# Kernel optimization log

Measured on AMD Instinct MI355X. Metric: run time of the kernel, lower is better.

The kernel has to match this reference:

```python
import jax, jax.numpy as jnp
import numpy as np

D_IN = 1024
D_OUT = 1024
N_HEADS = 16
HEAD_DIM = D_OUT // N_HEADS


def setup_inputs() -> dict:
    key = jax.random.key(0)
    ks = jax.random.split(key, 5)
    scale = 0.02
    x = jax.random.normal(ks[0], (2, 2048, D_IN), dtype=jnp.float32)
    Wq = jax.random.normal(ks[1], (D_IN, D_OUT), dtype=jnp.float32) * scale
    Wk = jax.random.normal(ks[2], (D_IN, D_OUT), dtype=jnp.float32) * scale
    Wv = jax.random.normal(ks[3], (D_IN, D_OUT), dtype=jnp.float32) * scale
    Wout = jax.random.normal(ks[4], (D_OUT, D_OUT), dtype=jnp.float32) * scale
    return {"x": x, "Wq": Wq, "Wk": Wk, "Wv": Wv, "Wout": Wout}


def reference(x, Wq, Wk, Wv, Wout):
    batch, seq_len, _ = x.shape
    # projections (no bias)
    Q = (x @ Wq).reshape(batch, seq_len, N_HEADS, HEAD_DIM)
    K = (x @ Wk).reshape(batch, seq_len, N_HEADS, HEAD_DIM)
    V = (x @ Wv).reshape(batch, seq_len, N_HEADS, HEAD_DIM)
    # scores: [batch, heads, seq, seq]
    scores = jnp.einsum("bqhd,bkhd->bhqk", Q, K) / jnp.sqrt(
        jnp.asarray(HEAD_DIM, dtype=x.dtype)
    )
    # causal mask: positions k > q masked to -inf
    causal = jnp.tril(jnp.ones((seq_len, seq_len), dtype=bool))
    scores = jnp.where(causal[None, None], scores, -jnp.inf)
    weights = jax.nn.softmax(scores, axis=-1)
    vectors = jnp.einsum("bhqk,bkhd->bqhd", weights, V)
    vectors = vectors.reshape(batch, seq_len, D_OUT)
    return vectors @ Wout
```

## Files before the change

kernel.cpp:

```cpp
#include <hip/hip_runtime.h>
#include <hip/hip_bf16.h>


typedef __attribute__((ext_vector_type(8))) _Float16 vhalf8;
typedef __attribute__((ext_vector_type(4))) _Float16 vhalf4;
typedef __attribute__((ext_vector_type(4))) float vfloat4;

#define D_MODEL 1024
#define SEQ     2048
#define NB      2
#define NH      16
#define HD      64

#define SCALE_K1 0.18033688f

__device__ __forceinline__ void async16(const void* g, void* l) {
  __builtin_amdgcn_global_load_lds(
      (const __attribute__((address_space(1))) unsigned int*)g,
      (__attribute__((address_space(3))) unsigned int*)l, 16, 0, 0);
}

__global__ __launch_bounds__(256) void prep(
    const float* __restrict__ x,
    const float* __restrict__ Wq, const float* __restrict__ Wk,
    const float* __restrict__ Wv, const float* __restrict__ Wo,
    _Float16* __restrict__ Xh, _Float16* __restrict__ Wt_qkv,
    _Float16* __restrict__ Wot) {
  int z = blockIdx.z;
  int t = threadIdx.x;
  if (z == 4) {
    int id = blockIdx.y * 16 + blockIdx.x;
#pragma unroll
    for (int pass = 0; pass < 8; pass++) {
      size_t i = ((size_t)(pass * 256 + id) * 256 + t) * 8;
      float4 a = *(const float4*)&x[i];
      float4 b = *(const float4*)&x[i + 4];
      vhalf8 h;
      h[0] = (_Float16)a.x; h[1] = (_Float16)a.y;
      h[2] = (_Float16)a.z; h[3] = (_Float16)a.w;
      h[4] = (_Float16)b.x; h[5] = (_Float16)b.y;
      h[6] = (_Float16)b.z; h[7] = (_Float16)b.w;
      *(vhalf8*)&Xh[i] = h;
    }
    return;
  }
  __shared__ _Float16 tile[64][65];
  const float* in = (z == 0) ? Wq : (z == 1) ? Wk : (z == 2) ? Wv : Wo;
  _Float16* out = (z < 3) ? (Wt_qkv + (size_t)z * 1024 * 1024) : Wot;
  int c0 = blockIdx.x * 64, r0 = blockIdx.y * 64;
  int tc = t & 63, tr = t >> 6;
#pragma unroll
  for (int p = 0; p < 16; p++) {
    int r = tr + p * 4;
    tile[r][tc] = (_Float16)in[(size_t)(r0 + r) * 1024 + c0 + tc];
  }
  __syncthreads();
#pragma unroll
  for (int p = 0; p < 16; p++) {
    int r = tr + p * 4;
    out[(size_t)(c0 + r) * 1024 + r0 + tc] = tile[tc][r];
  }
}

template <int BN>
__global__ __launch_bounds__(256) void gemm128(
    const _Float16* __restrict__ A, const _Float16* __restrict__ Bt,
    _Float16* __restrict__ Ch, float* __restrict__ Cf,
    _Float16* __restrict__ Vt, int M, int N, int K, int mode) {
  constexpr int ACH = 8;
  constexpr int BCH = BN / 16;
  constexpr int CPW = (ACH + BCH) / 4;
  constexpr int JN = BN / 32;
  __shared__ _Float16 As[128 * 32];
  __shared__ _Float16 Bs[BN * 32];
  int m0 = blockIdx.x * 128, n0 = blockIdx.y * BN;
  int t = threadIdx.x;
  int lane = t & 63, wave = t >> 6;
  int wm = (wave >> 1) * 64, wn = (wave & 1) * (BN / 2);
  int col = lane & 15, quad = lane >> 4;
  int srow = lane >> 2;
  int gcol = (((lane & 3) ^ (srow & 3)) << 3);

  vfloat4 acc[4][JN];
#pragma unroll
  for (int i = 0; i < 4; i++)
#pragma unroll
    for (int j = 0; j < JN; j++) {
      acc[i][j][0] = 0.f; acc[i][j][1] = 0.f;
      acc[i][j][2] = 0.f; acc[i][j][3] = 0.f;
    }

  int xq = (quad ^ (col & 3)) * 8;

  for (int k0 = 0; k0 < K; k0 += 32) {
    __syncthreads();
#pragma unroll
    for (int j = 0; j < CPW; j++) {
      int c = wave * CPW + j;
      if (c < ACH) {
        int row = c * 16 + srow;
        async16(&A[(size_t)(m0 + row) * K + k0 + gcol], &As[c * 512]);
      } else {
        int row = (c - ACH) * 16 + srow;
        async16(&Bt[(size_t)(n0 + row) * K + k0 + gcol], &Bs[(c - ACH) * 512]);
      }
    }
    __syncthreads();

    vhalf8 af[4], bf[JN];
#pragma unroll
    for (int i = 0; i < 4; i++)
      af[i] = *(const vhalf8*)&As[(wm + i * 16 + col) * 32 + xq];
#pragma unroll
    for (int j = 0; j < JN; j++)
      bf[j] = *(const vhalf8*)&Bs[(wn + j * 16 + col) * 32 + xq];
#pragma unroll
    for (int i = 0; i < 4; i++)
#pragma unroll
      for (int j = 0; j < JN; j++)
        acc[i][j] = __builtin_amdgcn_mfma_f32_16x16x32_f16(af[i], bf[j], acc[i][j], 0, 0, 0);
  }

  bool vmode = (mode == 2) && (n0 >= 2048);
#pragma unroll
  for (int i = 0; i < 4; i++)
#pragma unroll
    for (int j = 0; j < JN; j++) {
      if (vmode) {
        int n = n0 + wn + j * 16 + col;
        int nn = n - 2048;
        int hh = nn >> 6, dd = nn & 63;
        int m_base = m0 + wm + i * 16 + quad * 4;
        int bb = m_base >> 11, ss = m_base & 2047;
        vhalf4 pk;
        pk[0] = (_Float16)acc[i][j][0]; pk[1] = (_Float16)acc[i][j][1];
        pk[2] = (_Float16)acc[i][j][2]; pk[3] = (_Float16)acc[i][j][3];
        *(vhalf4*)&Vt[(((size_t)bb * NH + hh) * HD + dd) * SEQ + ss] = pk;
      } else {
#pragma unroll
        for (int r = 0; r < 4; r++) {
          int m = m0 + wm + i * 16 + quad * 4 + r;
          int n = n0 + wn + j * 16 + col;
          if (mode == 1)
            Cf[(size_t)m * N + n] = acc[i][j][r];
          else
            Ch[(size_t)m * N + n] = (_Float16)acc[i][j][r];
        }
      }
    }
}

__global__ __launch_bounds__(512) void attn(
    const _Float16* __restrict__ QKV, const _Float16* __restrict__ Vt,
    _Float16* __restrict__ Vec) {
  int blk = blockIdx.x;
  int pp = blk >> 5;
  int hb = blk & 31;
  int h = hb & 15;
  int b = hb >> 4;

  const _Float16* Qb  = QKV + (size_t)(b * SEQ) * 3072 + h * HD;
  const _Float16* Kb  = QKV + (size_t)(b * SEQ) * 3072 + 1024 + h * HD;
  const _Float16* Vtb = Vt + (size_t)(b * NH + h) * HD * SEQ;

  int t = threadIdx.x;
  int lane = t & 63, wave = t >> 6;
  int sw = wave & 3, hf = wave >> 2;
  int col = lane & 15, quad = lane >> 4;

  __shared__ _Float16 Ks[2][64][72];
  __shared__ _Float16 Vs[2][64][72];
  __shared__ _Float16 Ps[8][16][72];
  __shared__ float Om[64][65];
  __shared__ float Lm[64];

  int tl = t & 255;
  int srow = tl >> 2;
  int scol = (tl & 3) * 16;
  int kslot = ((srow & 3) << 4) + (srow >> 2);
  int kcol = scol ^ ((srow & 3) << 4);

  int tiles[2] = {31 - pp, pp};

  vhalf8 kr0, kr1, vr0, vr1;
  {
    const _Float16* kg = &Kb[(size_t)(hf * 64 + srow) * 3072 + scol];
    kr0 = *(const vhalf8*)kg; kr1 = *(const vhalf8*)(kg + 8);
    const _Float16* vg = &Vtb[(size_t)srow * SEQ + hf * 64 + scol];
    vr0 = *(const vhalf8*)vg; vr1 = *(const vhalf8*)(vg + 8);
  }

#pragma unroll
  for (int phase = 0; phase < 2; phase++) {
    int qt = tiles[phase];
    int q0 = qt * 64;
    int ntk = qt + 1;
    int J = (ntk + 1) >> 1;
    int wq0 = q0 + sw * 16;

    vhalf8 qf0 = *(const vhalf8*)&Qb[(size_t)(wq0 + col) * 3072 + quad * 8];
    vhalf8 qf1 = *(const vhalf8*)&Qb[(size_t)(wq0 + col) * 3072 + 32 + quad * 8];
#pragma unroll
    for (int i = 0; i < 8; i++) {
      qf0[i] = qf0[i] * (_Float16)SCALE_K1;
      qf1[i] = qf1[i] * (_Float16)SCALE_K1;
    }

    vfloat4 o[4];
#pragma unroll
    for (int i = 0; i < 4; i++) { o[i][0]=0.f; o[i][1]=0.f; o[i][2]=0.f; o[i][3]=0.f; }
    float lsum[4] = {0.f, 0.f, 0.f, 0.f};

    for (int j = 0; j < J; j++) {
      int ti = 2 * j + hf;
      bool active = (ti < ntk);
      int kb = ti * 64;
      if (active) {
        *(vhalf8*)&Ks[hf][kslot][kcol]     = kr0;
        *(vhalf8*)&Ks[hf][kslot][kcol + 8] = kr1;
        *(vhalf8*)&Vs[hf][srow][scol]      = vr0;
        *(vhalf8*)&Vs[hf][srow][scol + 8]  = vr1;
      }
      __syncthreads();

      {
        int tnext;
        if (phase == 0)
          tnext = (ti + 2 < ntk) ? (ti + 2) : hf;
        else
          tnext = (ti + 2 < ntk) ? (ti + 2) : ti;
        int kpf = tnext * 64;
        const _Float16* kg = &Kb[(size_t)(kpf + srow) * 3072 + scol];
        kr0 = *(const vhalf8*)kg; kr1 = *(const vhalf8*)(kg + 8);
        const _Float16* vg = &Vtb[(size_t)srow * SEQ + kpf + scol];
        vr0 = *(const vhalf8*)vg; vr1 = *(const vhalf8*)(vg + 8);
      }

      if (active) {
        vhalf8 kf[4][2];
#pragma unroll
        for (int hh = 0; hh < 4; hh++) {
          int swz = hh << 4;
          kf[hh][0] = *(const vhalf8*)&Ks[hf][hh * 16 + col][(quad * 8) ^ swz];
          kf[hh][1] = *(const vhalf8*)&Ks[hf][hh * 16 + col][(32 + quad * 8) ^ swz];
        }
        vfloat4 s[4];
#pragma unroll
        for (int hh = 0; hh < 4; hh++) {
          vfloat4 z; z[0]=0.f; z[1]=0.f; z[2]=0.f; z[3]=0.f;
          z = __builtin_amdgcn_mfma_f32_16x16x32_f16(qf0, kf[hh][0], z, 0, 0, 0);
          z = __builtin_amdgcn_mfma_f32_16x16x32_f16(qf1, kf[hh][1], z, 0, 0, 0);
          s[hh] = z;
        }
        bool diag = (kb + 63 > wq0);
#pragma unroll
        for (int r = 0; r < 4; r++) {
          int q = wq0 + quad * 4 + r;
          float p[4];
#pragma unroll
          for (int hh = 0; hh < 4; hh++) {
            float sc = s[hh][r];
            if (diag && (kb + 4 * col + hh > q)) sc = -1e30f;
            p[hh] = __builtin_exp2f(sc);
          }
          lsum[r] += (p[0] + p[1]) + (p[2] + p[3]);
          vhalf4 ph;
          ph[0] = (_Float16)p[0]; ph[1] = (_Float16)p[1];
          ph[2] = (_Float16)p[2]; ph[3] = (_Float16)p[3];
          *(vhalf4*)&Ps[wave][quad * 4 + r][4 * col] = ph;
        }
        __asm__ __volatile__("s_waitcnt lgkmcnt(0)" ::: "memory");
        vhalf8 pf0 = *(const vhalf8*)&Ps[wave][col][quad * 8];
        vhalf8 pf1 = *(const vhalf8*)&Ps[wave][col][32 + quad * 8];
#pragma unroll
        for (int tt = 0; tt < 4; tt++) {
          vhalf8 vf0 = *(const vhalf8*)&Vs[hf][tt * 16 + col][quad * 8];
          vhalf8 vf1 = *(const vhalf8*)&Vs[hf][tt * 16 + col][32 + quad * 8];
          o[tt] = __builtin_amdgcn_mfma_f32_16x16x32_f16(pf0, vf0, o[tt], 0, 0, 0);
          o[tt] = __builtin_amdgcn_mfma_f32_16x16x32_f16(pf1, vf1, o[tt], 0, 0, 0);
        }
      }
      __syncthreads();
    }

    float rs[4];
#pragma unroll
    for (int r = 0; r < 4; r++) {
      float v = lsum[r];
#pragma unroll
      for (int msk = 1; msk < 16; msk <<= 1) v += __shfl_xor(v, msk, 64);
      rs[r] = v;
    }
    if (hf == 1) {
#pragma unroll
      for (int tt = 0; tt < 4; tt++)
#pragma unroll
        for (int r = 0; r < 4; r++)
          Om[sw * 16 + quad * 4 + r][tt * 16 + col] = o[tt][r];
      if (col == 0)
#pragma unroll
        for (int r = 0; r < 4; r++)
          Lm[sw * 16 + quad * 4 + r] = rs[r];
    }
    __syncthreads();
    if (hf == 0) {
      float inv_l[4];
#pragma unroll
      for (int r = 0; r < 4; r++)
        inv_l[r] = 1.0f / (rs[r] + Lm[sw * 16 + quad * 4 + r]);
#pragma unroll
      for (int tt = 0; tt < 4; tt++)
#pragma unroll
        for (int r = 0; r < 4; r++) {
          int q = wq0 + quad * 4 + r;
          int d = tt * 16 + col;
          float ov = o[tt][r] + Om[sw * 16 + quad * 4 + r][tt * 16 + col];
          Vec[(size_t)(b * SEQ + q) * D_MODEL + h * HD + d] =
              (_Float16)(ov * inv_l[r]);
        }
    }
  }
}

extern "C" void kernel_launch(void* const* d_in, const int* in_sizes, int n_in,
                              void* d_out, int out_size, void* d_ws, size_t ws_size,
                              hipStream_t stream) {
  const float* x  = (const float*)d_in[0];
  const float* Wq = (const float*)d_in[1];
  const float* Wk = (const float*)d_in[2];
  const float* Wv = (const float*)d_in[3];
  const float* Wo = (const float*)d_in[4];
  float* out = (float*)d_out;

  char* ws = (char*)d_ws;
  _Float16* Xh     = (_Float16*)ws;
  _Float16* Wt_qkv = (_Float16*)(ws + 8388608);
  _Float16* Wot    = (_Float16*)(ws + 14680064);
  _Float16* QKV    = (_Float16*)(ws + 16777216);
  _Float16* Vt     = (_Float16*)(ws + 41943040);
  _Float16* Vec    = (_Float16*)(ws + 50331648);

  dim3 tb(256);
  prep<<<dim3(16, 16, 5), tb, 0, stream>>>(x, Wq, Wk, Wv, Wo, Xh, Wt_qkv, Wot);
  gemm128<128><<<dim3(32, 24), tb, 0, stream>>>(Xh, Wt_qkv, QKV, nullptr, Vt,
                                                4096, 3072, 1024, 2);
  attn<<<dim3(512), dim3(512), 0, stream>>>(QKV, Vt, Vec);
  gemm128<64><<<dim3(32, 16), tb, 0, stream>>>(Vec, Wot, nullptr, out, nullptr,
                                               4096, 1024, 1024, 1);
}
```

Baseline: 182.2 us.

## Halve attention block size, give each wave 32 query rows for K/V reuse

The attention kernel now runs 256 threads per block instead of 512. Each wave handles two 16-row query sub-tiles, so every K and V fragment read from LDS feeds twice as many MFMAs. The K tile buffer and the output-merge buffer now share LDS through a union to cut the footprint. In exchange, per-thread register pressure rises, each thread issues twice as many global loads, and an extra barrier is added between phases to protect the aliased LDS.

```diff
diff --git a/kernel.cpp b/kernel.cpp
--- a/kernel.cpp
+++ b/kernel.cpp
@@ -150,7 +150,7 @@
     }
 }
 
-__global__ __launch_bounds__(512) void attn(
+__global__ __launch_bounds__(256, 2) void attn(
     const _Float16* __restrict__ QKV, const _Float16* __restrict__ Vt,
     _Float16* __restrict__ Vec) {
   int blk = blockIdx.x;
@@ -165,29 +165,36 @@
 
   int t = threadIdx.x;
   int lane = t & 63, wave = t >> 6;
-  int sw = wave & 3, hf = wave >> 2;
+  int sw = wave & 1, hf = wave >> 1;
   int col = lane & 15, quad = lane >> 4;
 
-  __shared__ _Float16 Ks[2][64][72];
+  __shared__ union {
+    _Float16 Ks[2][64][72];
+    float    Om[64][65];
+  } su;
   __shared__ _Float16 Vs[2][64][72];
-  __shared__ _Float16 Ps[8][16][72];
-  __shared__ float Om[64][65];
+  __shared__ _Float16 Ps[4][32][72];
   __shared__ float Lm[64];
 
-  int tl = t & 255;
+  int tl = t & 127;
   int srow = tl >> 2;
   int scol = (tl & 3) * 16;
-  int kslot = ((srow & 3) << 4) + (srow >> 2);
+  int kslotA = ((srow & 3) << 4) + (srow >> 2);
+  int kslotB = kslotA + 8;
   int kcol = scol ^ ((srow & 3) << 4);
 
   int tiles[2] = {31 - pp, pp};
 
-  vhalf8 kr0, kr1, vr0, vr1;
+  vhalf8 krA0, krA1, krB0, krB1, vrA0, vrA1, vrB0, vrB1;
   {
     const _Float16* kg = &Kb[(size_t)(hf * 64 + srow) * 3072 + scol];
-    kr0 = *(const vhalf8*)kg; kr1 = *(const vhalf8*)(kg + 8);
+    krA0 = *(const vhalf8*)kg; krA1 = *(const vhalf8*)(kg + 8);
+    kg += (size_t)32 * 3072;
+    krB0 = *(const vhalf8*)kg; krB1 = *(const vhalf8*)(kg + 8);
     const _Float16* vg = &Vtb[(size_t)srow * SEQ + hf * 64 + scol];
-    vr0 = *(const vhalf8*)vg; vr1 = *(const vhalf8*)(vg + 8);
+    vrA0 = *(const vhalf8*)vg; vrA1 = *(const vhalf8*)(vg + 8);
+    vg += (size_t)32 * SEQ;
+    vrB0 = *(const vhalf8*)vg; vrB1 = *(const vhalf8*)(vg + 8);
   }
 
 #pragma unroll
@@ -196,30 +203,44 @@
     int q0 = qt * 64;
     int ntk = qt + 1;
     int J = (ntk + 1) >> 1;
-    int wq0 = q0 + sw * 16;
-
-    vhalf8 qf0 = *(const vhalf8*)&Qb[(size_t)(wq0 + col) * 3072 + quad * 8];
-    vhalf8 qf1 = *(const vhalf8*)&Qb[(size_t)(wq0 + col) * 3072 + 32 + quad * 8];
-#pragma unroll
-    for (int i = 0; i < 8; i++) {
-      qf0[i] = qf0[i] * (_Float16)SCALE_K1;
-      qf1[i] = qf1[i] * (_Float16)SCALE_K1;
-    }
-
-    vfloat4 o[4];
-#pragma unroll
-    for (int i = 0; i < 4; i++) { o[i][0]=0.f; o[i][1]=0.f; o[i][2]=0.f; o[i][3]=0.f; }
-    float lsum[4] = {0.f, 0.f, 0.f, 0.f};
+    int wq0 = q0 + sw * 32;
+
+    vhalf8 qf0[2], qf1[2];
+#pragma unroll
+    for (int qs = 0; qs < 2; qs++) {
+      const _Float16* qp = &Qb[(size_t)(wq0 + qs * 16 + col) * 3072 + quad * 8];
+      qf0[qs] = *(const vhalf8*)qp;
+      qf1[qs] = *(const vhalf8*)(qp + 32);
+#pragma unroll
+      for (int i = 0; i < 8; i++) {
+        qf0[qs][i] = qf0[qs][i] * (_Float16)SCALE_K1;
+        qf1[qs][i] = qf1[qs][i] * (_Float16)SCALE_K1;
+      }
+    }
+
+    vfloat4 o[2][4];
+#pragma unroll
+    for (int qs = 0; qs < 2; qs++)
+#pragma unroll
+      for (int i = 0; i < 4; i++) {
+        o[qs][i][0] = 0.f; o[qs][i][1] = 0.f;
+        o[qs][i][2] = 0.f; o[qs][i][3] = 0.f;
+      }
+    float lsum[2][4] = {{0.f, 0.f, 0.f, 0.f}, {0.f, 0.f, 0.f, 0.f}};
 
     for (int j = 0; j < J; j++) {
       int ti = 2 * j + hf;
       bool active = (ti < ntk);
       int kb = ti * 64;
       if (active) {
-        *(vhalf8*)&Ks[hf][kslot][kcol]     = kr0;
-        *(vhalf8*)&Ks[hf][kslot][kcol + 8] = kr1;
-        *(vhalf8*)&Vs[hf][srow][scol]      = vr0;
-        *(vhalf8*)&Vs[hf][srow][scol + 8]  = vr1;
+        *(vhalf8*)&su.Ks[hf][kslotA][kcol]     = krA0;
+        *(vhalf8*)&su.Ks[hf][kslotA][kcol + 8] = krA1;
+        *(vhalf8*)&su.Ks[hf][kslotB][kcol]     = krB0;
+        *(vhalf8*)&su.Ks[hf][kslotB][kcol + 8] = krB1;
+        *(vhalf8*)&Vs[hf][srow][scol]          = vrA0;
+        *(vhalf8*)&Vs[hf][srow][scol + 8]      = vrA1;
+        *(vhalf8*)&Vs[hf][srow + 32][scol]     = vrB0;
+        *(vhalf8*)&Vs[hf][srow + 32][scol + 8] = vrB1;
       }
       __syncthreads();
 
@@ -231,9 +252,13 @@
           tnext = (ti + 2 < ntk) ? (ti + 2) : ti;
         int kpf = tnext * 64;
         const _Float16* kg = &Kb[(size_t)(kpf + srow) * 3072 + scol];
-        kr0 = *(const vhalf8*)kg; kr1 = *(const vhalf8*)(kg + 8);
+        krA0 = *(const vhalf8*)kg; krA1 = *(const vhalf8*)(kg + 8);
+        kg += (size_t)32 * 3072;
+        krB0 = *(const vhalf8*)kg; krB1 = *(const vhalf8*)(kg + 8);
         const _Float16* vg = &Vtb[(size_t)srow * SEQ + kpf + scol];
-        vr0 = *(const vhalf8*)vg; vr1 = *(const vhalf8*)(vg + 8);
+        vrA0 = *(const vhalf8*)vg; vrA1 = *(const vhalf8*)(vg + 8);
+        vg += (size_t)32 * SEQ;
+        vrB0 = *(const vhalf8*)vg; vrB1 = *(const vhalf8*)(vg + 8);
       }
 
       if (active) {
@@ -241,84 +266,105 @@
 #pragma unroll
         for (int hh = 0; hh < 4; hh++) {
           int swz = hh << 4;
-          kf[hh][0] = *(const vhalf8*)&Ks[hf][hh * 16 + col][(quad * 8) ^ swz];
-          kf[hh][1] = *(const vhalf8*)&Ks[hf][hh * 16 + col][(32 + quad * 8) ^ swz];
-        }
-        vfloat4 s[4];
-#pragma unroll
-        for (int hh = 0; hh < 4; hh++) {
-          vfloat4 z; z[0]=0.f; z[1]=0.f; z[2]=0.f; z[3]=0.f;
-          z = __builtin_amdgcn_mfma_f32_16x16x32_f16(qf0, kf[hh][0], z, 0, 0, 0);
-          z = __builtin_amdgcn_mfma_f32_16x16x32_f16(qf1, kf[hh][1], z, 0, 0, 0);
-          s[hh] = z;
-        }
-        bool diag = (kb + 63 > wq0);
-#pragma unroll
-        for (int r = 0; r < 4; r++) {
-          int q = wq0 + quad * 4 + r;
-          float p[4];
+          kf[hh][0] = *(const vhalf8*)&su.Ks[hf][hh * 16 + col][(quad * 8) ^ swz];
+          kf[hh][1] = *(const vhalf8*)&su.Ks[hf][hh * 16 + col][(32 + quad * 8) ^ swz];
+        }
+#pragma unroll
+        for (int qs = 0; qs < 2; qs++) {
+          int wq = wq0 + qs * 16;
+          vfloat4 s[4];
 #pragma unroll
           for (int hh = 0; hh < 4; hh++) {
-            float sc = s[hh][r];
-            if (diag && (kb + 4 * col + hh > q)) sc = -1e30f;
-            p[hh] = __builtin_exp2f(sc);
+            vfloat4 z; z[0]=0.f; z[1]=0.f; z[2]=0.f; z[3]=0.f;
+            z = __builtin_amdgcn_mfma_f32_16x16x32_f16(qf0[qs], kf[hh][0], z, 0, 0, 0);
+            z = __builtin_amdgcn_mfma_f32_16x16x32_f16(qf1[qs], kf[hh][1], z, 0, 0, 0);
+            s[hh] = z;
           }
-          lsum[r] += (p[0] + p[1]) + (p[2] + p[3]);
-          vhalf4 ph;
-          ph[0] = (_Float16)p[0]; ph[1] = (_Float16)p[1];
-          ph[2] = (_Float16)p[2]; ph[3] = (_Float16)p[3];
-          *(vhalf4*)&Ps[wave][quad * 4 + r][4 * col] = ph;
+          bool diag = (kb + 63 > wq);
+#pragma unroll
+          for (int r = 0; r < 4; r++) {
+            int q = wq + quad * 4 + r;
+            float p[4];
+#pragma unroll
+            for (int hh = 0; hh < 4; hh++) {
+              float sc = s[hh][r];
+              if (diag && (kb + 4 * col + hh > q)) sc = -1e30f;
+              p[hh] = __builtin_exp2f(sc);
+            }
+            lsum[qs][r] += (p[0] + p[1]) + (p[2] + p[3]);
+            vhalf4 ph;
+            ph[0] = (_Float16)p[0]; ph[1] = (_Float16)p[1];
+            ph[2] = (_Float16)p[2]; ph[3] = (_Float16)p[3];
+            *(vhalf4*)&Ps[wave][qs * 16 + quad * 4 + r][4 * col] = ph;
+          }
         }
         __asm__ __volatile__("s_waitcnt lgkmcnt(0)" ::: "memory");
-        vhalf8 pf0 = *(const vhalf8*)&Ps[wave][col][quad * 8];
-        vhalf8 pf1 = *(const vhalf8*)&Ps[wave][col][32 + quad * 8];
+        vhalf8 pf0[2], pf1[2];
+#pragma unroll
+        for (int qs = 0; qs < 2; qs++) {
+          pf0[qs] = *(const vhalf8*)&Ps[wave][qs * 16 + col][quad * 8];
+          pf1[qs] = *(const vhalf8*)&Ps[wave][qs * 16 + col][32 + quad * 8];
+        }
 #pragma unroll
         for (int tt = 0; tt < 4; tt++) {
           vhalf8 vf0 = *(const vhalf8*)&Vs[hf][tt * 16 + col][quad * 8];
           vhalf8 vf1 = *(const vhalf8*)&Vs[hf][tt * 16 + col][32 + quad * 8];
-          o[tt] = __builtin_amdgcn_mfma_f32_16x16x32_f16(pf0, vf0, o[tt], 0, 0, 0);
-          o[tt] = __builtin_amdgcn_mfma_f32_16x16x32_f16(pf1, vf1, o[tt], 0, 0, 0);
+#pragma unroll
+          for (int qs = 0; qs < 2; qs++) {
+            o[qs][tt] = __builtin_amdgcn_mfma_f32_16x16x32_f16(pf0[qs], vf0, o[qs][tt], 0, 0, 0);
+            o[qs][tt] = __builtin_amdgcn_mfma_f32_16x16x32_f16(pf1[qs], vf1, o[qs][tt], 0, 0, 0);
+          }
         }
       }
       __syncthreads();
     }
 
-    float rs[4];
-#pragma unroll
-    for (int r = 0; r < 4; r++) {
-      float v = lsum[r];
-#pragma unroll
-      for (int msk = 1; msk < 16; msk <<= 1) v += __shfl_xor(v, msk, 64);
-      rs[r] = v;
-    }
+    float rs[2][4];
+#pragma unroll
+    for (int qs = 0; qs < 2; qs++)
+#pragma unroll
+      for (int r = 0; r < 4; r++) {
+        float v = lsum[qs][r];
+#pragma unroll
+        for (int msk = 1; msk < 16; msk <<= 1) v += __shfl_xor(v, msk, 64);
+        rs[qs][r] = v;
+      }
     if (hf == 1) {
 #pragma unroll
-      for (int tt = 0; tt < 4; tt++)
-#pragma unroll
-        for (int r = 0; r < 4; r++)
-          Om[sw * 16 + quad * 4 + r][tt * 16 + col] = o[tt][r];
-      if (col == 0)
-#pragma unroll
-        for (int r = 0; r < 4; r++)
-          Lm[sw * 16 + quad * 4 + r] = rs[r];
+      for (int qs = 0; qs < 2; qs++) {
+#pragma unroll
+        for (int tt = 0; tt < 4; tt++)
+#pragma unroll
+          for (int r = 0; r < 4; r++)
+            su.Om[sw * 32 + qs * 16 + quad * 4 + r][tt * 16 + col] = o[qs][tt][r];
+        if (col == 0)
+#pragma unroll
+          for (int r = 0; r < 4; r++)
+            Lm[sw * 32 + qs * 16 + quad * 4 + r] = rs[qs][r];
+      }
     }
     __syncthreads();
     if (hf == 0) {
-      float inv_l[4];
-#pragma unroll
-      for (int r = 0; r < 4; r++)
-        inv_l[r] = 1.0f / (rs[r] + Lm[sw * 16 + quad * 4 + r]);
-#pragma unroll
-      for (int tt = 0; tt < 4; tt++)
-#pragma unroll
-        for (int r = 0; r < 4; r++) {
-          int q = wq0 + quad * 4 + r;
-          int d = tt * 16 + col;
-          float ov = o[tt][r] + Om[sw * 16 + quad * 4 + r][tt * 16 + col];
-          Vec[(size_t)(b * SEQ + q) * D_MODEL + h * HD + d] =
-              (_Float16)(ov * inv_l[r]);
-        }
-    }
+#pragma unroll
+      for (int qs = 0; qs < 2; qs++) {
+        float inv_l[4];
+#pragma unroll
+        for (int r = 0; r < 4; r++)
+          inv_l[r] = 1.0f / (rs[qs][r] + Lm[sw * 32 + qs * 16 + quad * 4 + r]);
+#pragma unroll
+        for (int tt = 0; tt < 4; tt++)
+#pragma unroll
+          for (int r = 0; r < 4; r++) {
+            int q = wq0 + qs * 16 + quad * 4 + r;
+            int d = tt * 16 + col;
+            float ov = o[qs][tt][r] +
+                       su.Om[sw * 32 + qs * 16 + quad * 4 + r][tt * 16 + col];
+            Vec[(size_t)(b * SEQ + q) * D_MODEL + h * HD + d] =
+                (_Float16)(ov * inv_l[r]);
+          }
+      }
+    }
+    __syncthreads();
   }
 }
 
@@ -344,7 +390,7 @@
   prep<<<dim3(16, 16, 5), tb, 0, stream>>>(x, Wq, Wk, Wv, Wo, Xh, Wt_qkv, Wot);
   gemm128<128><<<dim3(32, 24), tb, 0, stream>>>(Xh, Wt_qkv, QKV, nullptr, Vt,
                                                 4096, 3072, 1024, 2);
-  attn<<<dim3(512), dim3(512), 0, stream>>>(QKV, Vt, Vec);
+  attn<<<dim3(512), dim3(256), 0, stream>>>(QKV, Vt, Vec);
   gemm128<64><<<dim3(32, 16), tb, 0, stream>>>(Vec, Wot, nullptr, out, nullptr,
                                                4096, 1024, 1024, 1);
 }
```

Result: slower. 197.1 us (+8.2%).

## Split attention into one block per query tile, drop KV split-merge

Applied to the files above, without the earlier changes.

The attention kernel no longer gives each 512-thread block a pair of query tiles (long plus short) with two wave halves splitting the key tiles and merging through shared memory. It now launches 1024 blocks of 256 threads, each handling a single query tile over all its key tiles, ordered longest-first in a zigzag to balance load. This removes the Om/Lm cross-half reduction and cuts shared memory, allowing more resident blocks per CU. The cost is a serial key loop per block with no intra-block split, and the loop runs twice as many iterations per wave.

```diff
diff --git a/kernel.cpp b/kernel.cpp
--- a/kernel.cpp
+++ b/kernel.cpp
@@ -150,176 +150,142 @@
     }
 }
 
-__global__ __launch_bounds__(512) void attn(
+__global__ __launch_bounds__(256, 4) void attn(
     const _Float16* __restrict__ QKV, const _Float16* __restrict__ Vt,
     _Float16* __restrict__ Vec) {
-  int blk = blockIdx.x;
-  int pp = blk >> 5;
-  int hb = blk & 31;
+  int g = blockIdx.x;
+  int qti = g >> 5;
+  int hb = g & 31;
   int h = hb & 15;
   int b = hb >> 4;
+  int jj = qti & 7, aa = qti >> 3;
+  int qt = (aa == 0) ? (31 - jj) : (aa == 1) ? (16 + jj)
+         : (aa == 2) ? (15 - jj) : jj;
 
   const _Float16* Qb  = QKV + (size_t)(b * SEQ) * 3072 + h * HD;
   const _Float16* Kb  = QKV + (size_t)(b * SEQ) * 3072 + 1024 + h * HD;
   const _Float16* Vtb = Vt + (size_t)(b * NH + h) * HD * SEQ;
 
   int t = threadIdx.x;
-  int lane = t & 63, wave = t >> 6;
-  int sw = wave & 3, hf = wave >> 2;
+  int lane = t & 63, sw = t >> 6;
   int col = lane & 15, quad = lane >> 4;
 
-  __shared__ _Float16 Ks[2][64][72];
-  __shared__ _Float16 Vs[2][64][72];
-  __shared__ _Float16 Ps[8][16][72];
-  __shared__ float Om[64][65];
-  __shared__ float Lm[64];
-
-  int tl = t & 255;
-  int srow = tl >> 2;
-  int scol = (tl & 3) * 16;
+  __shared__ _Float16 Ks[64][72];
+  __shared__ _Float16 Vs[64][72];
+  __shared__ _Float16 Ps[4][16][72];
+
+  int srow = t >> 2;
+  int scol = (t & 3) * 16;
   int kslot = ((srow & 3) << 4) + (srow >> 2);
   int kcol = scol ^ ((srow & 3) << 4);
 
-  int tiles[2] = {31 - pp, pp};
+  int q0 = qt * 64;
+  int ntk = qt + 1;
+  int wq0 = q0 + sw * 16;
 
   vhalf8 kr0, kr1, vr0, vr1;
   {
-    const _Float16* kg = &Kb[(size_t)(hf * 64 + srow) * 3072 + scol];
+    const _Float16* kg = &Kb[(size_t)srow * 3072 + scol];
     kr0 = *(const vhalf8*)kg; kr1 = *(const vhalf8*)(kg + 8);
-    const _Float16* vg = &Vtb[(size_t)srow * SEQ + hf * 64 + scol];
+    const _Float16* vg = &Vtb[(size_t)srow * SEQ + scol];
     vr0 = *(const vhalf8*)vg; vr1 = *(const vhalf8*)(vg + 8);
   }
 
-#pragma unroll
-  for (int phase = 0; phase < 2; phase++) {
-    int qt = tiles[phase];
-    int q0 = qt * 64;
-    int ntk = qt + 1;
-    int J = (ntk + 1) >> 1;
-    int wq0 = q0 + sw * 16;
-
-    vhalf8 qf0 = *(const vhalf8*)&Qb[(size_t)(wq0 + col) * 3072 + quad * 8];
-    vhalf8 qf1 = *(const vhalf8*)&Qb[(size_t)(wq0 + col) * 3072 + 32 + quad * 8];
-#pragma unroll
-    for (int i = 0; i < 8; i++) {
-      qf0[i] = qf0[i] * (_Float16)SCALE_K1;
-      qf1[i] = qf1[i] * (_Float16)SCALE_K1;
-    }
-
-    vfloat4 o[4];
-#pragma unroll
-    for (int i = 0; i < 4; i++) { o[i][0]=0.f; o[i][1]=0.f; o[i][2]=0.f; o[i][3]=0.f; }
-    float lsum[4] = {0.f, 0.f, 0.f, 0.f};
-
-    for (int j = 0; j < J; j++) {
-      int ti = 2 * j + hf;
-      bool active = (ti < ntk);
-      int kb = ti * 64;
-      if (active) {
-        *(vhalf8*)&Ks[hf][kslot][kcol]     = kr0;
-        *(vhalf8*)&Ks[hf][kslot][kcol + 8] = kr1;
-        *(vhalf8*)&Vs[hf][srow][scol]      = vr0;
-        *(vhalf8*)&Vs[hf][srow][scol + 8]  = vr1;
+  vhalf8 qf0 = *(const vhalf8*)&Qb[(size_t)(wq0 + col) * 3072 + quad * 8];
+  vhalf8 qf1 = *(const vhalf8*)&Qb[(size_t)(wq0 + col) * 3072 + 32 + quad * 8];
+#pragma unroll
+  for (int i = 0; i < 8; i++) {
+    qf0[i] = qf0[i] * (_Float16)SCALE_K1;
+    qf1[i] = qf1[i] * (_Float16)SCALE_K1;
+  }
+
+  vfloat4 o[4];
+#pragma unroll
+  for (int i = 0; i < 4; i++) { o[i][0]=0.f; o[i][1]=0.f; o[i][2]=0.f; o[i][3]=0.f; }
+  float lsum[4] = {0.f, 0.f, 0.f, 0.f};
+
+  for (int ti = 0; ti < ntk; ti++) {
+    int kb = ti * 64;
+    *(vhalf8*)&Ks[kslot][kcol]     = kr0;
+    *(vhalf8*)&Ks[kslot][kcol + 8] = kr1;
+    *(vhalf8*)&Vs[srow][scol]      = vr0;
+    *(vhalf8*)&Vs[srow][scol + 8]  = vr1;
+    __syncthreads();
+
+    {
+      int tnext = (ti + 1 < ntk) ? (ti + 1) : ti;
+      int kpf = tnext * 64;
+      const _Float16* kg = &Kb[(size_t)(kpf + srow) * 3072 + scol];
+      kr0 = *(const vhalf8*)kg; kr1 = *(const vhalf8*)(kg + 8);
+      const _Float16* vg = &Vtb[(size_t)srow * SEQ + kpf + scol];
+      vr0 = *(const vhalf8*)vg; vr1 = *(const vhalf8*)(vg + 8);
+    }
+
+    vhalf8 kf[4][2];
+#pragma unroll
+    for (int hh = 0; hh < 4; hh++) {
+      int swz = hh << 4;
+      kf[hh][0] = *(const vhalf8*)&Ks[hh * 16 + col][(quad * 8) ^ swz];
+      kf[hh][1] = *(const vhalf8*)&Ks[hh * 16 + col][(32 + quad * 8) ^ swz];
+    }
+    vfloat4 s[4];
+#pragma unroll
+    for (int hh = 0; hh < 4; hh++) {
+      vfloat4 z; z[0]=0.f; z[1]=0.f; z[2]=0.f; z[3]=0.f;
+      z = __builtin_amdgcn_mfma_f32_16x16x32_f16(qf0, kf[hh][0], z, 0, 0, 0);
+      z = __builtin_amdgcn_mfma_f32_16x16x32_f16(qf1, kf[hh][1], z, 0, 0, 0);
+      s[hh] = z;
+    }
+    bool diag = (kb + 63 > wq0);
+#pragma unroll
+    for (int r = 0; r < 4; r++) {
+      int q = wq0 + quad * 4 + r;
+      float p[4];
+#pragma unroll
+      for (int hh = 0; hh < 4; hh++) {
+        float sc = s[hh][r];
+        if (diag && (kb + 4 * col + hh > q)) sc = -1e30f;
+        p[hh] = __builtin_exp2f(sc);
       }
-      __syncthreads();
-
-      {
-        int tnext;
-        if (phase == 0)
-          tnext = (ti + 2 < ntk) ? (ti + 2) : hf;
-        else
-          tnext = (ti + 2 < ntk) ? (ti + 2) : ti;
-        int kpf = tnext * 64;
-        const _Float16* kg = &Kb[(size_t)(kpf + srow) * 3072 + scol];
-        kr0 = *(const vhalf8*)kg; kr1 = *(const vhalf8*)(kg + 8);
-        const _Float16* vg = &Vtb[(size_t)srow * SEQ + kpf + scol];
-        vr0 = *(const vhalf8*)vg; vr1 = *(const vhalf8*)(vg + 8);
-      }
-
-      if (active) {
-        vhalf8 kf[4][2];
-#pragma unroll
-        for (int hh = 0; hh < 4; hh++) {
-          int swz = hh << 4;
-          kf[hh][0] = *(const vhalf8*)&Ks[hf][hh * 16 + col][(quad * 8) ^ swz];
-          kf[hh][1] = *(const vhalf8*)&Ks[hf][hh * 16 + col][(32 + quad * 8) ^ swz];
-        }
-        vfloat4 s[4];
-#pragma unroll
-        for (int hh = 0; hh < 4; hh++) {
-          vfloat4 z; z[0]=0.f; z[1]=0.f; z[2]=0.f; z[3]=0.f;
-          z = __builtin_amdgcn_mfma_f32_16x16x32_f16(qf0, kf[hh][0], z, 0, 0, 0);
-          z = __builtin_amdgcn_mfma_f32_16x16x32_f16(qf1, kf[hh][1], z, 0, 0, 0);
-          s[hh] = z;
-        }
-        bool diag = (kb + 63 > wq0);
-#pragma unroll
-        for (int r = 0; r < 4; r++) {
-          int q = wq0 + quad * 4 + r;
-          float p[4];
-#pragma unroll
-          for (int hh = 0; hh < 4; hh++) {
-            float sc = s[hh][r];
-            if (diag && (kb + 4 * col + hh > q)) sc = -1e30f;
-            p[hh] = __builtin_exp2f(sc);
-          }
-          lsum[r] += (p[0] + p[1]) + (p[2] + p[3]);
-          vhalf4 ph;
-          ph[0] = (_Float16)p[0]; ph[1] = (_Float16)p[1];
-          ph[2] = (_Float16)p[2]; ph[3] = (_Float16)p[3];
-          *(vhalf4*)&Ps[wave][quad * 4 + r][4 * col] = ph;
-        }
-        __asm__ __volatile__("s_waitcnt lgkmcnt(0)" ::: "memory");
-        vhalf8 pf0 = *(const vhalf8*)&Ps[wave][col][quad * 8];
-        vhalf8 pf1 = *(const vhalf8*)&Ps[wave][col][32 + quad * 8];
-#pragma unroll
-        for (int tt = 0; tt < 4; tt++) {
-          vhalf8 vf0 = *(const vhalf8*)&Vs[hf][tt * 16 + col][quad * 8];
-          vhalf8 vf1 = *(const vhalf8*)&Vs[hf][tt * 16 + col][32 + quad * 8];
-          o[tt] = __builtin_amdgcn_mfma_f32_16x16x32_f16(pf0, vf0, o[tt], 0, 0, 0);
-          o[tt] = __builtin_amdgcn_mfma_f32_16x16x32_f16(pf1, vf1, o[tt], 0, 0, 0);
-        }
-      }
-      __syncthreads();
-    }
-
-    float rs[4];
+      lsum[r] += (p[0] + p[1]) + (p[2] + p[3]);
+      vhalf4 ph;
+      ph[0] = (_Float16)p[0]; ph[1] = (_Float16)p[1];
+      ph[2] = (_Float16)p[2]; ph[3] = (_Float16)p[3];
+      *(vhalf4*)&Ps[sw][quad * 4 + r][4 * col] = ph;
+    }
+    __asm__ __volatile__("s_waitcnt lgkmcnt(0)" ::: "memory");
+    vhalf8 pf0 = *(const vhalf8*)&Ps[sw][col][quad * 8];
+    vhalf8 pf1 = *(const vhalf8*)&Ps[sw][col][32 + quad * 8];
+#pragma unroll
+    for (int tt = 0; tt < 4; tt++) {
+      vhalf8 vf0 = *(const vhalf8*)&Vs[tt * 16 + col][quad * 8];
+      vhalf8 vf1 = *(const vhalf8*)&Vs[tt * 16 + col][32 + quad * 8];
+      o[tt] = __builtin_amdgcn_mfma_f32_16x16x32_f16(pf0, vf0, o[tt], 0, 0, 0);
+      o[tt] = __builtin_amdgcn_mfma_f32_16x16x32_f16(pf1, vf1, o[tt], 0, 0, 0);
+    }
+    __syncthreads();
+  }
+
+  float rs[4];
+#pragma unroll
+  for (int r = 0; r < 4; r++) {
+    float v = lsum[r];
+#pragma unroll
+    for (int msk = 1; msk < 16; msk <<= 1) v += __shfl_xor(v, msk, 64);
+    rs[r] = v;
+  }
+  float inv_l[4];
+#pragma unroll
+  for (int r = 0; r < 4; r++) inv_l[r] = 1.0f / rs[r];
+#pragma unroll
+  for (int tt = 0; tt < 4; tt++)
 #pragma unroll
     for (int r = 0; r < 4; r++) {
-      float v = lsum[r];
-#pragma unroll
-      for (int msk = 1; msk < 16; msk <<= 1) v += __shfl_xor(v, msk, 64);
-      rs[r] = v;
-    }
-    if (hf == 1) {
-#pragma unroll
-      for (int tt = 0; tt < 4; tt++)
-#pragma unroll
-        for (int r = 0; r < 4; r++)
-          Om[sw * 16 + quad * 4 + r][tt * 16 + col] = o[tt][r];
-      if (col == 0)
-#pragma unroll
-        for (int r = 0; r < 4; r++)
-          Lm[sw * 16 + quad * 4 + r] = rs[r];
-    }
-    __syncthreads();
-    if (hf == 0) {
-      float inv_l[4];
-#pragma unroll
-      for (int r = 0; r < 4; r++)
-        inv_l[r] = 1.0f / (rs[r] + Lm[sw * 16 + quad * 4 + r]);
-#pragma unroll
-      for (int tt = 0; tt < 4; tt++)
-#pragma unroll
-        for (int r = 0; r < 4; r++) {
-          int q = wq0 + quad * 4 + r;
-          int d = tt * 16 + col;
-          float ov = o[tt][r] + Om[sw * 16 + quad * 4 + r][tt * 16 + col];
-          Vec[(size_t)(b * SEQ + q) * D_MODEL + h * HD + d] =
-              (_Float16)(ov * inv_l[r]);
-        }
-    }
-  }
+      int q = wq0 + quad * 4 + r;
+      int d = tt * 16 + col;
+      Vec[(size_t)(b * SEQ + q) * D_MODEL + h * HD + d] =
+          (_Float16)(o[tt][r] * inv_l[r]);
+    }
 }
 
 extern "C" void kernel_launch(void* const* d_in, const int* in_sizes, int n_in,
@@ -344,7 +310,7 @@
   prep<<<dim3(16, 16, 5), tb, 0, stream>>>(x, Wq, Wk, Wv, Wo, Xh, Wt_qkv, Wot);
   gemm128<128><<<dim3(32, 24), tb, 0, stream>>>(Xh, Wt_qkv, QKV, nullptr, Vt,
                                                 4096, 3072, 1024, 2);
-  attn<<<dim3(512), dim3(512), 0, stream>>>(QKV, Vt, Vec);
+  attn<<<dim3(1024), dim3(256), 0, stream>>>(QKV, Vt, Vec);
   gemm128<64><<<dim3(32, 16), tb, 0, stream>>>(Vec, Wot, nullptr, out, nullptr,
                                                4096, 1024, 1024, 1);
 }
```

Result: faster. 177.5 us (-2.6%).
